# Performance work log

Hardware: AMD Instinct MI355X
Metric: run time of the kernel (lower is better)

The kernel has to match this reference:

```python
import jax, jax.numpy as jnp
import numpy as np

BS, T, D_IN = 128, 32, 128
DH = 128          # controller hidden size == memory word width M
N_SLOTS = 512     # memory rows
EPS = 1e-8


def _split_read(o):
    # o: [bs, M+6] -> k, beta, g, s(3), gamma
    k = o[:, :DH]
    beta = jax.nn.softplus(o[:, DH])
    g = jax.nn.sigmoid(o[:, DH + 1])
    s = jax.nn.softmax(o[:, DH + 2:DH + 5], axis=-1)
    gamma = 1.0 + jax.nn.softplus(o[:, DH + 5])
    return k, beta, g, s, gamma


def _attention(k, beta, g, s, gamma, mem, w_prev):
    # content addressing: cosine similarity sharpened by beta
    dot = jnp.einsum('bnm,bm->bn', mem, k)
    denom = jnp.linalg.norm(mem, axis=-1) * jnp.linalg.norm(k, axis=-1, keepdims=True) + EPS
    w_c = jax.nn.softmax(beta[:, None] * dot / denom, axis=-1)
    # gate interpolation with previous weights
    w_g = g[:, None] * w_c + (1.0 - g[:, None]) * w_prev
    # circular shift convolution over offsets {-1, 0, +1}
    w_t = (s[:, 0:1] * jnp.roll(w_g, -1, axis=-1)
           + s[:, 1:2] * w_g
           + s[:, 2:3] * jnp.roll(w_g, 1, axis=-1))
    # sharpening
    w = w_t ** gamma[:, None]
    return w / (jnp.sum(w, axis=-1, keepdims=True) + EPS)


def setup_inputs() -> dict:
    key = jax.random.key(0)
    ks = jax.random.split(key, 8)
    sc = lambda fan_in: 1.0 / np.sqrt(fan_in)
    return {
        'x':    jax.random.normal(ks[0], (BS, T, D_IN), jnp.float32),
        'Wxh':  jax.random.normal(ks[1], (D_IN, DH), jnp.float32) * sc(D_IN),
        'Whh':  jax.random.normal(ks[2], (DH, DH), jnp.float32) * sc(DH),
        'Wrh':  jax.random.normal(ks[3], (DH, DH), jnp.float32) * sc(DH),
        'bh':   jnp.zeros((DH,), jnp.float32),
        'Wout': jax.random.normal(ks[4], (DH + DH, D_IN), jnp.float32) * sc(2 * DH),
        'bout': jnp.zeros((D_IN,), jnp.float32),
        'Wr':   jax.random.normal(ks[5], (DH, DH + 6), jnp.float32) * sc(DH),
        'br':   jnp.zeros((DH + 6,), jnp.float32),
        'Ww':   jax.random.normal(ks[6], (DH, 3 * DH + 6), jnp.float32) * sc(DH),
        'bw':   jnp.zeros((3 * DH + 6,), jnp.float32),
    }


def reference(x, Wxh, Whh, Wrh, bh, Wout, bout, Wr, br, Ww, bw):
    bs = x.shape[0]
    h0 = jnp.zeros((bs, DH), x.dtype)
    r0 = jnp.zeros((bs, DH), x.dtype)
    w0 = jnp.full((bs, N_SLOTS), 1.0 / N_SLOTS, x.dtype)
    mem0 = jnp.full((bs, N_SLOTS, DH), 1e-6, x.dtype)

    def step(carry, x_t):
        h, r, w_prev, mem = carry
        # controller state
        h = jnp.tanh(x_t @ Wxh + h @ Whh + r @ Wrh + bh)
        # head parameter projections
        o_r = h @ Wr + br
        o_w = h @ Ww + bw
        k_r, b_r, g_r, s_r, y_r = _split_read(o_r)
        k_w, b_w_, g_w, s_w, y_w = _split_read(o_w[:, :DH + 6])
        e = jax.nn.sigmoid(o_w[:, DH + 6:2 * DH + 6])   # erase [bs, M]
        a = jnp.tanh(o_w[:, 2 * DH + 6:3 * DH + 6])     # add   [bs, M]
        # addressing (w_previous updated sequentially, read then write)
        w_r = _attention(k_r, b_r, g_r, s_r, y_r, mem, w_prev)
        w_w = _attention(k_w, b_w_, g_w, s_w, y_w, mem, w_r)
        # read
        r = jnp.einsum('bn,bnm->bm', w_r, mem)
        # erase / add write
        mem = mem * (1.0 - w_w[:, :, None] * e[:, None, :]) + w_w[:, :, None] * a[:, None, :]
        # output
        y = jnp.concatenate([h, r], axis=-1) @ Wout + bout
        return (h, r, w_w, mem), y

    _, ys = jax.lax.scan(step, (h0, r0, w0, mem0), jnp.swapaxes(x, 0, 1))
    return jnp.swapaxes(ys, 0, 1)  # [bs, ft, d_output]
```

## Files before the change

kernel.cpp:

```cpp
#include <hip/hip_runtime.h>
#include <hip/hip_bf16.h>
#include <math.h>

#define NT 1024
#define BSZ 128
#define TSTEPS 32
#define DIN 128
#define DHH 128
#define NSLOT 512
#define EPSF 1e-8f

static constexpr int F_FLOATS = 7160;
static constexpr size_t LDS_BYTES = 131072 + F_FLOATS * sizeof(float);

__device__ __forceinline__ float bf_lo(unsigned u) {
  union { unsigned u; float f; } c; c.u = u << 16; return c.f;
}
__device__ __forceinline__ float bf_hi(unsigned u) {
  union { unsigned u; float f; } c; c.u = u & 0xffff0000u; return c.f;
}
__device__ __forceinline__ unsigned short f2us(float f) {
  union { unsigned short s; __hip_bfloat16 h; } c; c.h = __float2bfloat16(f); return c.s;
}
__device__ __forceinline__ unsigned pkbf(float a, float b) {
  union { __hip_bfloat162 h2; unsigned u; } c;
  c.h2 = __float22bfloat162_rn(make_float2(a, b));
  return c.u;
}
__device__ __forceinline__ float sigmoid_(float x) { return 1.0f / (1.0f + __expf(-x)); }
__device__ __forceinline__ float softplus_(float x) {
  return fmaxf(x, 0.0f) + log1pf(__expf(-fabsf(x)));
}
__device__ __forceinline__ float tanh_(float x) {
  float e = __expf(-2.0f * fabsf(x));
  float t = (1.0f - e) / (1.0f + e);
  return copysignf(t, x);
}
__device__ __forceinline__ float waveSum(float v) {
#pragma unroll
  for (int m = 32; m >= 1; m >>= 1) v += __shfl_xor(v, m);
  return v;
}

__device__ __forceinline__ void bar_lds() {
  asm volatile("s_waitcnt lgkmcnt(0)" ::: "memory");
  __builtin_amdgcn_s_barrier();
}

__global__ __launch_bounds__(NT, 4)
void ntm_kernel(const float* __restrict__ x,
                const float* __restrict__ Wxh,
                const float* __restrict__ Whh,
                const float* __restrict__ Wrh,
                const float* __restrict__ bh,
                const float* __restrict__ Wout,
                const float* __restrict__ bout,
                const float* __restrict__ Wr,
                const float* __restrict__ br,
                const float* __restrict__ Ww,
                const float* __restrict__ bw,
                float* __restrict__ out)
{
  extern __shared__ char smem[];
  uint4* memv = (uint4*)smem;
  float* F = (float*)(smem + 131072);

  const int b = blockIdx.x;
  const int tid = threadIdx.x;
  const int g = tid >> 4, l = tid & 15;
  const int lane = tid & 63, wid = tid >> 6;

  float* U      = F + 0;
  float* yP     = F + 2560;
  float* sWprev = F + 4608;
  float* sWr    = F + 5120;
  float* sP1    = F + 5632;
  float* sOr    = F + 6144;
  float* sOw    = F + 6288;
  float* sXt    = F + 6680;
  float* sH     = F + 6808;
  float* sR     = F + 6936;
  float* sP     = F + 7064;
  float* V      = sXt;
  uint4* krP    = (uint4*)(sP1 + 0);
  uint4* kwP    = (uint4*)(sP1 + 64);
  float* eR     = U + 0;
  float* eW     = U + 512;

  {
    const unsigned short mb = f2us(1e-6f);
    const unsigned w32 = ((unsigned)mb << 16) | mb;
    const uint4 fv = make_uint4(w32, w32, w32, w32);
    for (int i = tid; i < NSLOT * DHH / 8; i += NT) memv[i] = fv;
  }
  for (int i = tid; i < NSLOT; i += NT) sWprev[i] = 1.0f / NSLOT;
  if (tid < DHH) { sH[tid] = 0.0f; sR[tid] = 0.0f; }
  if (tid < DIN) sXt[tid] = x[(size_t)b * TSTEPS * DIN + tid];
  __syncthreads();

  for (int t = 0; t < TSTEPS; ++t) {
    {
      const int q = tid & 63, s = tid >> 6;
      const int j2 = q * 2, i0 = s * 24;
      float2 acc = make_float2(0.f, 0.f);
#pragma unroll 2
      for (int k = 0; k < 6; ++k) {
        const float4 vv = *(const float4*)(V + i0 + 4 * k);
        const float vk[4] = { vv.x, vv.y, vv.z, vv.w };
#pragma unroll
        for (int u = 0; u < 4; ++u) {
          const int i = i0 + 4 * k + u;
          const float* Wp = (i < 128) ? (Wxh + i * DHH)
                          : (i < 256) ? (Whh + (i - 128) * DHH)
                                      : (Wrh + (i - 256) * DHH);
          const float2 wv = *(const float2*)(Wp + j2);
          acc.x = fmaf(vk[u], wv.x, acc.x);
          acc.y = fmaf(vk[u], wv.y, acc.y);
        }
      }
      *(float2*)(U + s * 128 + j2) = acc;
      bar_lds();
    }
    if (tid < DHH) {
      float a2 = bh[tid];
#pragma unroll
      for (int q2 = 0; q2 < 16; ++q2) a2 += U[q2 * 128 + tid];
      sH[tid] = tanh_(a2);
    }
    bar_lds();

    {
      {
        const int s = tid;
        const int q = (s >= 786) ? 3 : (s >= 524) ? 2 : (s >= 262) ? 1 : 0;
        const int P = s - 262 * q;
        const int i0 = 32 * q;
        const float2* p;
        int strideF2;
        if (P < 67) { p = (const float2*)(Wr + i0 * 134 + 2 * P); strideF2 = 67; }
        else        { p = (const float2*)(Ww + i0 * 390 + 2 * (P - 67)); strideF2 = 195; }
        float2 acc = make_float2(0.f, 0.f);
#pragma unroll 2
        for (int k = 0; k < 8; ++k) {
          const float4 hv = *(const float4*)(sH + i0 + 4 * k);
          const float hk[4] = { hv.x, hv.y, hv.z, hv.w };
#pragma unroll
          for (int u = 0; u < 4; ++u) {
            const float2 wv = p[(4 * k + u) * strideF2];
            acc.x = fmaf(hk[u], wv.x, acc.x);
            acc.y = fmaf(hk[u], wv.y, acc.y);
          }
        }
        *(float2*)(U + s * 2) = acc;
      }
      if (lane < 3) {
        const int hs = wid * 3 + lane;
        const int e = hs >> 1, hh = hs & 1;
        const int cp = 171 + e;
        const int i0 = 96 + 16 * hh;
        const float2* p = (const float2*)(Ww + i0 * 390 + 2 * cp);
        float2 acc = make_float2(0.f, 0.f);
#pragma unroll 8
        for (int w = 0; w < 16; ++w) {
          const float v = sH[i0 + w];
          const float2 wv = *p;
          acc.x = fmaf(v, wv.x, acc.x);
          acc.y = fmaf(v, wv.y, acc.y);
          p += 195;
        }
        U[2096 + hs * 2]     = acc.x;
        U[2096 + hs * 2 + 1] = acc.y;
      }
      if (tid == 1023) {
        sP[0] = 0.f; sP[1] = 0.f; sP[2] = 0.f; sP[3] = 0.f; sP[4] = 0.f; sP[5] = 0.f;
      }
      bar_lds();
    }

    {
      if (tid < 134) {
        float v = 0.f;
#pragma unroll
        for (int q = 0; q < 4; ++q) v += U[tid + 524 * q];
        v += br[tid];
        sOr[tid] = v;
        if (tid < 128) {
          float s2 = waveSum(v * v);
          if (lane == 0) atomicAdd(&sP[0], s2);
        }
      } else if (tid == 134) {
        float sc[6];
#pragma unroll
        for (int j = 0; j < 6; ++j) {
          float v = 0.f;
#pragma unroll
          for (int q = 0; q < 4; ++q) v += U[(128 + j) + 524 * q];
          sc[j] = v + br[128 + j];
        }
        sP[80] = softplus_(sc[0]);
        sP[81] = sigmoid_(sc[1]);
        float mx = fmaxf(sc[2], fmaxf(sc[3], sc[4]));
        float e0 = __expf(sc[2] - mx), e1 = __expf(sc[3] - mx), e2 = __expf(sc[4] - mx);
        float es = e0 + e1 + e2;
        sP[82] = e0 / es; sP[83] = e1 / es; sP[84] = e2 / es;
        sP[85] = 1.0f + softplus_(sc[5]);
      } else if (tid == 135) {
        float sc[6];
#pragma unroll
        for (int j = 0; j < 6; ++j) {
          float v = 0.f;
#pragma unroll
          for (int q = 0; q < 4; ++q) v += U[(262 + j) + 524 * q];
          sc[j] = v + bw[128 + j];
        }
        sP[86] = softplus_(sc[0]);
        sP[87] = sigmoid_(sc[1]);
        float mx = fmaxf(sc[2], fmaxf(sc[3], sc[4]));
        float e0 = __expf(sc[2] - mx), e1 = __expf(sc[3] - mx), e2 = __expf(sc[4] - mx);
        float es = e0 + e1 + e2;
        sP[88] = e0 / es; sP[89] = e1 / es; sP[90] = e2 / es;
        sP[91] = 1.0f + softplus_(sc[5]);
      } else if (tid >= 256 && tid < 512) {
        const int cc = tid + 12;
        float v = U[cc] + U[cc + 524] + U[cc + 1048];
        if (cc < 476) {
          v += U[cc + 1572];
        } else {
          const int cw = cc - 134;
          const int e = (cw >> 1) - 171;
          const int base = 2096 + 4 * e + (cw & 1);
          v += U[base] + U[base + 2];
        }
        v += bw[tid - 122];
        sOw[tid - 120] = (tid < 384) ? sigmoid_(v) : tanh_(v);
      } else if (tid >= 512 && tid < 640) {
        const int cw = tid - 512;
        float v = 0.f;
#pragma unroll
        for (int q = 0; q < 4; ++q) v += U[(134 + cw) + 524 * q];
        v += bw[cw];
        sOw[cw] = v;
        float s2 = waveSum(v * v);
        if (lane == 0) atomicAdd(&sP[1], s2);
      } else if (tid >= 640 && tid < 768) {
        sR[tid - 640] = 0.f;
      } else if (tid >= 768 && tid < 800) {
        const int t2 = tid - 768;
        const int c = t2 & 15;
        union { uint4 v; unsigned short h[8]; } pk;
#pragma unroll
        for (int j = 0; j < 8; ++j) {
          const int col = c * 8 + j;
          float v = 0.f;
#pragma unroll
          for (int q = 0; q < 4; ++q)
            v += U[((t2 < 16) ? col : (134 + col)) + 524 * q];
          v += (t2 < 16) ? br[col] : bw[col];
          pk.h[j] = f2us(v);
        }
        if (t2 < 16) krP[c] = pk.v; else kwP[c] = pk.v;
      } else if (tid >= 896) {
        if (t > 0) {
          const int c = tid - 896;
          float y = bout[c];
#pragma unroll
          for (int q = 0; q < 16; ++q) y += yP[q * 128 + c];
          out[((size_t)b * TSTEPS + (t - 1)) * DIN + c] = y;
        }
      }
      bar_lds();
    }

    {
      const float kn_r = sqrtf(sP[0]);
      const float kn_w = sqrtf(sP[1]);
      const float beta_r = sP[80], beta_w = sP[86];
      const int n = tid >> 1, hf = tid & 1;
      const int sw = (n >> 2) & 3;
      float dr = 0.f, dw = 0.f, ss = 0.f;
#pragma unroll
      for (int c = 0; c < 8; ++c) {
        const int cl = hf * 8 + c;
        const uint4 mv = memv[n * 16 + (cl ^ sw)];
        const uint4 kr = krP[cl];
        const uint4 kw = kwP[cl];
        const unsigned mw_[4] = { mv.x, mv.y, mv.z, mv.w };
        const unsigned krw[4] = { kr.x, kr.y, kr.z, kr.w };
        const unsigned kww[4] = { kw.x, kw.y, kw.z, kw.w };
#pragma unroll
        for (int j = 0; j < 4; ++j) {
          const float m0 = bf_lo(mw_[j]), m1 = bf_hi(mw_[j]);
          dr = fmaf(m0, bf_lo(krw[j]), dr); dr = fmaf(m1, bf_hi(krw[j]), dr);
          dw = fmaf(m0, bf_lo(kww[j]), dw); dw = fmaf(m1, bf_hi(kww[j]), dw);
          ss = fmaf(m0, m0, ss);            ss = fmaf(m1, m1, ss);
        }
      }
      dr += __shfl_xor(dr, 1);
      dw += __shfl_xor(dw, 1);
      ss += __shfl_xor(ss, 1);
      const float nr = sqrtf(ss);
      const float er = __expf(beta_r * dr / (nr * kn_r + EPSF));
      const float ew = __expf(beta_w * dw / (nr * kn_w + EPSF));
      if (hf == 0) { eR[n] = er; eW[n] = ew; }
      float s1 = waveSum(er) * 0.5f;
      float s2 = waveSum(ew) * 0.5f;
      if (lane == 0) { atomicAdd(&sP[2], s1); atomicAdd(&sP[3], s2); }
      bar_lds();
    }

    {
      if (tid < NSLOT) {
        const float invE = 1.0f / sP[2];
        const float gr = sP[81], omg = 1.0f - sP[81];
        const int im = (tid - 1) & 511, ip = (tid + 1) & 511;
        const float wgm = gr * (eR[im] * invE) + omg * sWprev[im];
        const float wg0 = gr * (eR[tid] * invE) + omg * sWprev[tid];
        const float wgp = gr * (eR[ip] * invE) + omg * sWprev[ip];
        const float wt = sP[82] * wgp + sP[83] * wg0 + sP[84] * wgm;
        float p1 = (wt > 0.0f) ? __expf(sP[85] * __logf(wt)) : 0.0f;
        float P = waveSum(p1);
        sP1[tid] = p1;
        if (lane == 0) atomicAdd(&sP[4], P);
      } else {
        const int p = tid - 512;
        const int j4 = (p & 31) * 4, sl = p >> 5;
        float4 acc = make_float4(0.f, 0.f, 0.f, 0.f);
#pragma unroll
        for (int w = 0; w < 8; ++w) {
          const float v = sH[8 * sl + w];
          const float4 wv = *(const float4*)(Wout + (8 * sl + w) * DIN + j4);
          acc.x = fmaf(v, wv.x, acc.x); acc.y = fmaf(v, wv.y, acc.y);
          acc.z = fmaf(v, wv.z, acc.z); acc.w = fmaf(v, wv.w, acc.w);
        }
        *(float4*)(yP + sl * 128 + j4) = acc;
      }
      bar_lds();
    }
    {
      if (tid < NSLOT) {
        const float pinv1 = 1.0f / (sP[4] + EPSF);
        const float invE = 1.0f / sP[3];
        const float gw = sP[87], omg = 1.0f - sP[87];
        const int im = (tid - 1) & 511, ip = (tid + 1) & 511;
        const float wgm = gw * (eW[im] * invE) + omg * (sP1[im] * pinv1);
        const float wg0 = gw * (eW[tid] * invE) + omg * (sP1[tid] * pinv1);
        const float wgp = gw * (eW[ip] * invE) + omg * (sP1[ip] * pinv1);
        sWr[tid] = sP1[tid] * pinv1;
        const float wt = sP[88] * wgp + sP[89] * wg0 + sP[90] * wgm;
        float p2 = (wt > 0.0f) ? __expf(sP[91] * __logf(wt)) : 0.0f;
        float P = waveSum(p2);
        U[tid] = p2;
        if (lane == 0) atomicAdd(&sP[5], P);
      } else if (tid < 512 + DIN && t + 1 < TSTEPS) {
        const int i = tid - 512;
        sXt[i] = x[((size_t)b * TSTEPS + (t + 1)) * DIN + i];
      }
      bar_lds();
    }

    {
      const float pinv2 = 1.0f / (sP[5] + EPSF);
      if (tid < NSLOT) sWprev[tid] = U[tid] * pinv2;

      const int cl = l ^ ((g >> 2) & 3);
      float4 e4a = *(const float4*)(sOw + 136 + cl * 8);
      float4 e4b = *(const float4*)(sOw + 140 + cl * 8);
      float4 a4a = *(const float4*)(sOw + 264 + cl * 8);
      float4 a4b = *(const float4*)(sOw + 268 + cl * 8);
      const float e8[8] = { e4a.x, e4a.y, e4a.z, e4a.w, e4b.x, e4b.y, e4b.z, e4b.w };
      const float a8[8] = { a4a.x, a4a.y, a4a.z, a4a.w, a4b.x, a4b.y, a4b.z, a4b.w };
      float r8[8] = { 0, 0, 0, 0, 0, 0, 0, 0 };
#pragma unroll 2
      for (int it = 0; it < 8; ++it) {
        const int n = g + 64 * it;
        const float wrn = sWr[n];
        const float wwn = U[n] * pinv2;
        uint4 pk = memv[n * 16 + l];
        const unsigned wds[4] = { pk.x, pk.y, pk.z, pk.w };
        float m[8];
#pragma unroll
        for (int j = 0; j < 4; ++j) { m[2 * j] = bf_lo(wds[j]); m[2 * j + 1] = bf_hi(wds[j]); }
#pragma unroll
        for (int j = 0; j < 8; ++j) {
          r8[j] = fmaf(wrn, m[j], r8[j]);
          const float d = fmaf(-e8[j], m[j], a8[j]);
          m[j] = fmaf(wwn, d, m[j]);
        }
        pk.x = pkbf(m[0], m[1]);
        pk.y = pkbf(m[2], m[3]);
        pk.z = pkbf(m[4], m[5]);
        pk.w = pkbf(m[6], m[7]);
        memv[n * 16 + l] = pk;
      }
#pragma unroll
      for (int j = 0; j < 8; ++j) {
        r8[j] += __shfl_xor(r8[j], 16);
        r8[j] += __shfl_xor(r8[j], 32);
      }
      if (lane < 16) {
#pragma unroll
        for (int j = 0; j < 8; ++j) atomicAdd(&sR[cl * 8 + j], r8[j]);
      }
      bar_lds();
    }

    {
      if (tid < 512) {
        const int j4 = (tid & 31) * 4, sl = tid >> 5;
        float4 acc = *(const float4*)(yP + sl * 128 + j4);
#pragma unroll
        for (int w = 0; w < 8; ++w) {
          const float v = sR[8 * sl + w];
          const float4 wv = *(const float4*)(Wout + (128 + 8 * sl + w) * DIN + j4);
          acc.x = fmaf(v, wv.x, acc.x); acc.y = fmaf(v, wv.y, acc.y);
          acc.z = fmaf(v, wv.z, acc.z); acc.w = fmaf(v, wv.w, acc.w);
        }
        *(float4*)(yP + sl * 128 + j4) = acc;
      }
      bar_lds();
    }
  }

  if (tid < DIN) {
    float y = bout[tid];
#pragma unroll
    for (int q = 0; q < 16; ++q) y += yP[q * 128 + tid];
    out[((size_t)b * TSTEPS + (TSTEPS - 1)) * DIN + tid] = y;
  }
}

extern "C" void kernel_launch(void* const* d_in, const int* in_sizes, int n_in,
                              void* d_out, int out_size, void* d_ws, size_t ws_size,
                              hipStream_t stream) {
  (void)in_sizes; (void)n_in; (void)out_size; (void)d_ws; (void)ws_size;
  hipFuncSetAttribute(reinterpret_cast<const void*>(ntm_kernel),
                      hipFuncAttributeMaxDynamicSharedMemorySize, (int)LDS_BYTES);
  ntm_kernel<<<dim3(BSZ), dim3(NT), LDS_BYTES, stream>>>(
      (const float*)d_in[0], (const float*)d_in[1], (const float*)d_in[2],
      (const float*)d_in[3], (const float*)d_in[4], (const float*)d_in[5],
      (const float*)d_in[6], (const float*)d_in[7], (const float*)d_in[8],
      (const float*)d_in[9], (const float*)d_in[10],
      (float*)d_out);
}
```

Before: 852.6 us.

## Split each batch's memory across two workgroups with global-memory handshakes

Each batch element is now handled by two workgroups, each owning half of the 512 memory slots (256 rows) in LDS. The 128 workgroups of the old launch leave most CUs idle, so this doubles the number of CUs working and halves per-block LDS and memory-row work. Partial softmax sums, boundary weights for the circular shift, and read-vector partials are exchanged through a global workspace, using flag spinning four times per timestep. The cost is cross-CU synchronisation latency on every step, and the code relies on both blocks of a pair being co-resident, or it deadlocks.

```diff
diff --git a/kernel.cpp b/kernel.cpp
--- a/kernel.cpp
+++ b/kernel.cpp
@@ -8,10 +8,19 @@
 #define DIN 128
 #define DHH 128
 #define NSLOT 512
+#define NMY 256
 #define EPSF 1e-8f
 
 static constexpr int F_FLOATS = 7160;
-static constexpr size_t LDS_BYTES = 131072 + F_FLOATS * sizeof(float);
+static constexpr size_t LDS_BYTES = 65536 + F_FLOATS * sizeof(float);
+
+#define WSTRIDE 512
+#define S1OFF 0
+#define S2OFF 32
+#define S3OFF 34
+#define S4R   64
+#define S4P   320
+#define FLG   352
 
 __device__ __forceinline__ float bf_lo(unsigned u) {
   union { unsigned u; float f; } c; c.u = u << 16; return c.f;
@@ -41,10 +50,15 @@
   for (int m = 32; m >= 1; m >>= 1) v += __shfl_xor(v, m);
   return v;
 }
-
 __device__ __forceinline__ void bar_lds() {
   asm volatile("s_waitcnt lgkmcnt(0)" ::: "memory");
   __builtin_amdgcn_s_barrier();
+}
+__device__ __forceinline__ void st_ws(float* p, float v) {
+  __hip_atomic_store(p, v, __ATOMIC_RELAXED, __HIP_MEMORY_SCOPE_AGENT);
+}
+__device__ __forceinline__ float ld_ws(const float* p) {
+  return __hip_atomic_load(p, __ATOMIC_RELAXED, __HIP_MEMORY_SCOPE_AGENT);
 }
 
 __global__ __launch_bounds__(NT, 4)
@@ -59,13 +73,16 @@
                 const float* __restrict__ br,
                 const float* __restrict__ Ww,
                 const float* __restrict__ bw,
+                float* __restrict__ ws,
                 float* __restrict__ out)
 {
   extern __shared__ char smem[];
   uint4* memv = (uint4*)smem;
-  float* F = (float*)(smem + 131072);
-
-  const int b = blockIdx.x;
+  float* F = (float*)(smem + 65536);
+
+  const int b    = blockIdx.x & 127;
+  const int half = blockIdx.x >> 7;
+  const int s0   = half * NMY;
   const int tid = threadIdx.x;
   const int g = tid >> 4, l = tid & 15;
   const int lane = tid & 63, wid = tid >> 6;
@@ -87,11 +104,18 @@
   float* eR     = U + 0;
   float* eW     = U + 512;
 
+  float* WS = ws + (size_t)b * WSTRIDE;
+  unsigned* flg = (unsigned*)(WS + FLG);
+  const int tg0 = (s0 + 256) & 511;
+  const int tg1 = (s0 + 257) & 511;
+  const int tg2 = (s0 + 510) & 511;
+  const int tg3 = (s0 + 511) & 511;
+
   {
     const unsigned short mb = f2us(1e-6f);
     const unsigned w32 = ((unsigned)mb << 16) | mb;
     const uint4 fv = make_uint4(w32, w32, w32, w32);
-    for (int i = tid; i < NSLOT * DHH / 8; i += NT) memv[i] = fv;
+    for (int i = tid; i < NMY * DHH / 8; i += NT) memv[i] = fv;
   }
   for (int i = tid; i < NSLOT; i += NT) sWprev[i] = 1.0f / NSLOT;
   if (tid < DHH) { sH[tid] = 0.0f; sR[tid] = 0.0f; }
@@ -259,9 +283,9 @@
           pk.h[j] = f2us(v);
         }
         if (t2 < 16) krP[c] = pk.v; else kwP[c] = pk.v;
-      } else if (tid >= 896) {
+      } else if (tid >= 896 && tid < 960) {
         if (t > 0) {
-          const int c = tid - 896;
+          const int c = half * 64 + (tid - 896);
           float y = bout[c];
 #pragma unroll
           for (int q = 0; q < 16; ++q) y += yP[q * 128 + c];
@@ -275,13 +299,14 @@
       const float kn_r = sqrtf(sP[0]);
       const float kn_w = sqrtf(sP[1]);
       const float beta_r = sP[80], beta_w = sP[86];
-      const int n = tid >> 1, hf = tid & 1;
-      const int sw = (n >> 2) & 3;
+      const int nl = tid >> 2, qf = tid & 3;
+      const int n  = s0 + nl;
+      const int sw = (nl >> 2) & 3;
       float dr = 0.f, dw = 0.f, ss = 0.f;
 #pragma unroll
-      for (int c = 0; c < 8; ++c) {
-        const int cl = hf * 8 + c;
-        const uint4 mv = memv[n * 16 + (cl ^ sw)];
+      for (int c = 0; c < 4; ++c) {
+        const int cl = qf * 4 + c;
+        const uint4 mv = memv[nl * 16 + (cl ^ sw)];
         const uint4 kr = krP[cl];
         const uint4 kw = kwP[cl];
         const unsigned mw_[4] = { mv.x, mv.y, mv.z, mv.w };
@@ -295,35 +320,73 @@
           ss = fmaf(m0, m0, ss);            ss = fmaf(m1, m1, ss);
         }
       }
-      dr += __shfl_xor(dr, 1);
-      dw += __shfl_xor(dw, 1);
-      ss += __shfl_xor(ss, 1);
+      dr += __shfl_xor(dr, 1); dr += __shfl_xor(dr, 2);
+      dw += __shfl_xor(dw, 1); dw += __shfl_xor(dw, 2);
+      ss += __shfl_xor(ss, 1); ss += __shfl_xor(ss, 2);
       const float nr = sqrtf(ss);
       const float er = __expf(beta_r * dr / (nr * kn_r + EPSF));
       const float ew = __expf(beta_w * dw / (nr * kn_w + EPSF));
-      if (hf == 0) { eR[n] = er; eW[n] = ew; }
-      float s1 = waveSum(er) * 0.5f;
-      float s2 = waveSum(ew) * 0.5f;
-      if (lane == 0) { atomicAdd(&sP[2], s1); atomicAdd(&sP[3], s2); }
-      bar_lds();
-    }
-
-    {
-      if (tid < NSLOT) {
+      if (qf == 0) { eR[n] = er; eW[n] = ew; }
+      float s1_ = waveSum((qf == 0) ? er : 0.f);
+      float s2_ = waveSum((qf == 0) ? ew : 0.f);
+      if (lane == 0) { atomicAdd(&sP[2], s1_); atomicAdd(&sP[3], s2_); }
+      bar_lds();
+    }
+
+    {
+      const unsigned tok = (unsigned)(t * 4 + 1);
+      float* myb = WS + S1OFF + half * 16;
+      if (tid < 10) {
+        float v;
+        if (tid == 0)      v = sP[2];
+        else if (tid == 1) v = sP[3];
+        else if (tid < 6)  { const int k = tid - 2; v = eR[s0 + ((k < 2) ? k : k + 252)]; }
+        else               { const int k = tid - 6; v = eW[s0 + ((k < 2) ? k : k + 252)]; }
+        st_ws(myb + tid, v);
+        __threadfence();
+      }
+      __builtin_amdgcn_s_barrier();
+      if (tid == 0) {
+        __hip_atomic_store(&flg[half], tok, __ATOMIC_RELEASE, __HIP_MEMORY_SCOPE_AGENT);
+        while (__hip_atomic_load(&flg[1 - half], __ATOMIC_ACQUIRE, __HIP_MEMORY_SCOPE_AGENT) < tok)
+          __builtin_amdgcn_s_sleep(1);
+      }
+      __builtin_amdgcn_s_barrier();
+      float* ob = WS + S1OFF + (1 - half) * 16;
+      if (tid < 10) {
+        const float pv = ld_ws(ob + tid);
+        if (tid == 0)      { const float my = sP[2]; sP[2] = half ? (pv + my) : (my + pv); }
+        else if (tid == 1) { const float my = sP[3]; sP[3] = half ? (pv + my) : (my + pv); }
+        else if (tid == 2) eR[tg0] = pv;
+        else if (tid == 3) eR[tg1] = pv;
+        else if (tid == 4) eR[tg2] = pv;
+        else if (tid == 5) eR[tg3] = pv;
+        else if (tid == 6) eW[tg0] = pv;
+        else if (tid == 7) eW[tg1] = pv;
+        else if (tid == 8) eW[tg2] = pv;
+        else               eW[tg3] = pv;
+      }
+      bar_lds();
+    }
+
+    {
+      if (tid < 320) {
+        const bool av = (tid < 258);
+        const int nn = (s0 - 1 + tid) & 511;
         const float invE = 1.0f / sP[2];
         const float gr = sP[81], omg = 1.0f - sP[81];
-        const int im = (tid - 1) & 511, ip = (tid + 1) & 511;
+        const int im = (nn - 1) & 511, ip = (nn + 1) & 511;
         const float wgm = gr * (eR[im] * invE) + omg * sWprev[im];
-        const float wg0 = gr * (eR[tid] * invE) + omg * sWprev[tid];
+        const float wg0 = gr * (eR[nn] * invE) + omg * sWprev[nn];
         const float wgp = gr * (eR[ip] * invE) + omg * sWprev[ip];
         const float wt = sP[82] * wgp + sP[83] * wg0 + sP[84] * wgm;
         float p1 = (wt > 0.0f) ? __expf(sP[85] * __logf(wt)) : 0.0f;
-        float P = waveSum(p1);
-        sP1[tid] = p1;
+        float P = waveSum((tid >= 1 && tid <= 256) ? p1 : 0.f);
+        if (av) sP1[nn] = p1;
         if (lane == 0) atomicAdd(&sP[4], P);
-      } else {
+      } else if (tid >= 512 && tid < 768) {
         const int p = tid - 512;
-        const int j4 = (p & 31) * 4, sl = p >> 5;
+        const int j4 = (p & 15) * 4 + half * 64, sl = p >> 4;
         float4 acc = make_float4(0.f, 0.f, 0.f, 0.f);
 #pragma unroll
         for (int w = 0; w < 8; ++w) {
@@ -336,22 +399,39 @@
       }
       bar_lds();
     }
-    {
-      if (tid < NSLOT) {
+
+    {
+      const unsigned tok = (unsigned)(t * 4 + 2);
+      if (tid == 0) {
+        const float my = sP[4];
+        st_ws(WS + S2OFF + half, my);
+        __threadfence();
+        __hip_atomic_store(&flg[half], tok, __ATOMIC_RELEASE, __HIP_MEMORY_SCOPE_AGENT);
+        while (__hip_atomic_load(&flg[1 - half], __ATOMIC_ACQUIRE, __HIP_MEMORY_SCOPE_AGENT) < tok)
+          __builtin_amdgcn_s_sleep(1);
+        const float pv = ld_ws(WS + S2OFF + (1 - half));
+        sP[4] = half ? (pv + my) : (my + pv);
+      }
+      bar_lds();
+    }
+
+    {
+      if (tid < NMY) {
+        const int n = s0 + tid;
         const float pinv1 = 1.0f / (sP[4] + EPSF);
         const float invE = 1.0f / sP[3];
         const float gw = sP[87], omg = 1.0f - sP[87];
-        const int im = (tid - 1) & 511, ip = (tid + 1) & 511;
+        const int im = (n - 1) & 511, ip = (n + 1) & 511;
         const float wgm = gw * (eW[im] * invE) + omg * (sP1[im] * pinv1);
-        const float wg0 = gw * (eW[tid] * invE) + omg * (sP1[tid] * pinv1);
+        const float wg0 = gw * (eW[n] * invE) + omg * (sP1[n] * pinv1);
         const float wgp = gw * (eW[ip] * invE) + omg * (sP1[ip] * pinv1);
-        sWr[tid] = sP1[tid] * pinv1;
+        sWr[n] = sP1[n] * pinv1;
         const float wt = sP[88] * wgp + sP[89] * wg0 + sP[90] * wgm;
         float p2 = (wt > 0.0f) ? __expf(sP[91] * __logf(wt)) : 0.0f;
         float P = waveSum(p2);
-        U[tid] = p2;
+        U[n] = p2;
         if (lane == 0) atomicAdd(&sP[5], P);
-      } else if (tid < 512 + DIN && t + 1 < TSTEPS) {
+      } else if (tid >= 512 && tid < 512 + DIN && t + 1 < TSTEPS) {
         const int i = tid - 512;
         sXt[i] = x[((size_t)b * TSTEPS + (t + 1)) * DIN + i];
       }
@@ -359,8 +439,23 @@
     }
 
     {
+      const unsigned tok = (unsigned)(t * 4 + 3);
+      if (tid == 0) {
+        const float my = sP[5];
+        st_ws(WS + S3OFF + half, my);
+        __threadfence();
+        __hip_atomic_store(&flg[half], tok, __ATOMIC_RELEASE, __HIP_MEMORY_SCOPE_AGENT);
+        while (__hip_atomic_load(&flg[1 - half], __ATOMIC_ACQUIRE, __HIP_MEMORY_SCOPE_AGENT) < tok)
+          __builtin_amdgcn_s_sleep(1);
+        const float pv = ld_ws(WS + S3OFF + (1 - half));
+        sP[5] = half ? (pv + my) : (my + pv);
+      }
+      bar_lds();
+    }
+
+    {
       const float pinv2 = 1.0f / (sP[5] + EPSF);
-      if (tid < NSLOT) sWprev[tid] = U[tid] * pinv2;
+      if (tid < NMY) sWprev[s0 + tid] = U[s0 + tid] * pinv2;
 
       const int cl = l ^ ((g >> 2) & 3);
       float4 e4a = *(const float4*)(sOw + 136 + cl * 8);
@@ -371,11 +466,12 @@
       const float a8[8] = { a4a.x, a4a.y, a4a.z, a4a.w, a4b.x, a4b.y, a4b.z, a4b.w };
       float r8[8] = { 0, 0, 0, 0, 0, 0, 0, 0 };
 #pragma unroll 2
-      for (int it = 0; it < 8; ++it) {
-        const int n = g + 64 * it;
+      for (int it = 0; it < 4; ++it) {
+        const int nl = g + 64 * it;
+        const int n  = s0 + nl;
         const float wrn = sWr[n];
         const float wwn = U[n] * pinv2;
-        uint4 pk = memv[n * 16 + l];
+        uint4 pk = memv[nl * 16 + l];
         const unsigned wds[4] = { pk.x, pk.y, pk.z, pk.w };
         float m[8];
 #pragma unroll
@@ -390,7 +486,7 @@
         pk.y = pkbf(m[2], m[3]);
         pk.z = pkbf(m[4], m[5]);
         pk.w = pkbf(m[6], m[7]);
-        memv[n * 16 + l] = pk;
+        memv[nl * 16 + l] = pk;
       }
 #pragma unroll
       for (int j = 0; j < 8; ++j) {
@@ -405,8 +501,40 @@
     }
 
     {
-      if (tid < 512) {
-        const int j4 = (tid & 31) * 4, sl = tid >> 5;
+      const unsigned tok = (unsigned)(t * 4 + 4);
+      float myr = 0.f;
+      if (tid < 128) {
+        myr = sR[tid];
+        st_ws(WS + S4R + half * 128 + tid, myr);
+        __threadfence();
+      } else if (tid < 132) {
+        const int k = tid - 128;
+        st_ws(WS + S4P + half * 4 + k, U[s0 + ((k < 2) ? k : k + 252)]);
+        __threadfence();
+      }
+      __builtin_amdgcn_s_barrier();
+      if (tid == 0) {
+        __hip_atomic_store(&flg[half], tok, __ATOMIC_RELEASE, __HIP_MEMORY_SCOPE_AGENT);
+        while (__hip_atomic_load(&flg[1 - half], __ATOMIC_ACQUIRE, __HIP_MEMORY_SCOPE_AGENT) < tok)
+          __builtin_amdgcn_s_sleep(1);
+      }
+      __builtin_amdgcn_s_barrier();
+      if (tid < 128) {
+        const float pv = ld_ws(WS + S4R + (1 - half) * 128 + tid);
+        sR[tid] = half ? (pv + myr) : (myr + pv);
+      } else if (tid < 132) {
+        const int k = tid - 128;
+        const float pv = ld_ws(WS + S4P + (1 - half) * 4 + k);
+        const float pinv2 = 1.0f / (sP[5] + EPSF);
+        const int tgt = (k == 0) ? tg0 : (k == 1) ? tg1 : (k == 2) ? tg2 : tg3;
+        sWprev[tgt] = pv * pinv2;
+      }
+      bar_lds();
+    }
+
+    {
+      if (tid < 256) {
+        const int j4 = (tid & 15) * 4 + half * 64, sl = tid >> 4;
         float4 acc = *(const float4*)(yP + sl * 128 + j4);
 #pragma unroll
         for (int w = 0; w < 8; ++w) {
@@ -421,24 +549,26 @@
     }
   }
 
-  if (tid < DIN) {
-    float y = bout[tid];
-#pragma unroll
-    for (int q = 0; q < 16; ++q) y += yP[q * 128 + tid];
-    out[((size_t)b * TSTEPS + (TSTEPS - 1)) * DIN + tid] = y;
+  if (tid < 64) {
+    const int c = half * 64 + tid;
+    float y = bout[c];
+#pragma unroll
+    for (int q = 0; q < 16; ++q) y += yP[q * 128 + c];
+    out[((size_t)b * TSTEPS + (TSTEPS - 1)) * DIN + c] = y;
   }
 }
 
 extern "C" void kernel_launch(void* const* d_in, const int* in_sizes, int n_in,
                               void* d_out, int out_size, void* d_ws, size_t ws_size,
                               hipStream_t stream) {
-  (void)in_sizes; (void)n_in; (void)out_size; (void)d_ws; (void)ws_size;
+  (void)in_sizes; (void)n_in; (void)out_size; (void)ws_size;
   hipFuncSetAttribute(reinterpret_cast<const void*>(ntm_kernel),
                       hipFuncAttributeMaxDynamicSharedMemorySize, (int)LDS_BYTES);
-  ntm_kernel<<<dim3(BSZ), dim3(NT), LDS_BYTES, stream>>>(
+  hipMemsetAsync(d_ws, 0, (size_t)BSZ * WSTRIDE * sizeof(float), stream);
+  ntm_kernel<<<dim3(2 * BSZ), dim3(NT), LDS_BYTES, stream>>>(
       (const float*)d_in[0], (const float*)d_in[1], (const float*)d_in[2],
       (const float*)d_in[3], (const float*)d_in[4], (const float*)d_in[5],
       (const float*)d_in[6], (const float*)d_in[7], (const float*)d_in[8],
       (const float*)d_in[9], (const float*)d_in[10],
-      (float*)d_out);
-}
+      (float*)d_ws, (float*)d_out);
+}
```

New measurement: 1.865 ms. +118.8%, slower.
